# Optimization experiments

Measured on AMD Instinct MI355X. Metric: run time of the kernel, lower is better.

The kernel has to match this reference:

```python
import jax, jax.numpy as jnp
import numpy as np


def setup_inputs() -> dict:
    key = jax.random.key(0)
    ks = jax.random.split(key, 11)
    B, D, H = 2048, 1024, 1024
    return {
        "x": jax.random.normal(ks[0], (B, D), jnp.float32),
        "h_prev": jax.random.normal(ks[1], (B, H), jnp.float32),
        "W_mu": jax.random.normal(ks[2], (D, 3 * H), jnp.float32) * 0.05,
        "W_rho": jax.random.normal(ks[3], (D, 3 * H), jnp.float32) - 4.0,
        "U_mu": jax.random.normal(ks[4], (H, 3 * H), jnp.float32) * 0.05,
        "U_rho": jax.random.normal(ks[5], (H, 3 * H), jnp.float32) - 4.0,
        "b_mu": jax.random.normal(ks[6], (3 * H,), jnp.float32) * 0.05,
        "b_rho": jax.random.normal(ks[7], (3 * H,), jnp.float32) - 4.0,
        "r_eps": jax.random.normal(ks[8], (H,), jnp.float32),
        "u_eps": jax.random.normal(ks[9], (H,), jnp.float32),
        "h_pre_eps": jax.random.normal(ks[10], (H,), jnp.float32),
    }


def reference(x, h_prev, W_mu, W_rho, U_mu, U_rho, b_mu, b_rho,
              r_eps, u_eps, h_pre_eps):
    # Local reparameterization GRU cell (Bayes-by-Backprop).
    # Fused mean path: [B, 3H]
    mu = x @ W_mu + h_prev @ U_mu + b_mu
    # Variance path: E[x]^2 with sigma = softplus(rho); note original adds
    # b_sig (not squared) as in the source code.
    W_sig2 = jnp.square(jax.nn.softplus(W_rho))
    U_sig2 = jnp.square(jax.nn.softplus(U_rho))
    b_sig = jax.nn.softplus(b_rho)
    sig = jnp.square(x) @ W_sig2 + jnp.square(h_prev) @ U_sig2 + b_sig

    H = h_prev.shape[1]
    mu_r, mu_u, mu_h = mu[:, :H], mu[:, H:2 * H], mu[:, 2 * H:]
    sig_r, sig_u, sig_h = sig[:, :H], sig[:, H:2 * H], sig[:, 2 * H:]

    r = jax.nn.sigmoid(mu_r + sig_r * r_eps)  # computed as in source (unused in local path h update)
    u = jax.nn.sigmoid(mu_u + sig_u * u_eps)
    h_pre = jnp.tanh(mu_h + sig_h * h_pre_eps)
    h = u * h_prev + (1.0 - u) * h_pre
    return h
```

## Files before the change

kernel.cpp:

```cpp
#include <hip/hip_runtime.h>
#include <stdint.h>

#define BB 2048
#define DD 1024
#define HH 1024
#define KK 4096
#define NN 2048

typedef __bf16 bf16x8 __attribute__((ext_vector_type(8)));
typedef float  f32x4  __attribute__((ext_vector_type(4)));
typedef unsigned short u16x8 __attribute__((ext_vector_type(8)));

__device__ __forceinline__ unsigned short f2bf(float f) {
  union { float f; uint32_t u; } v; v.f = f;
  uint32_t r = (v.u + 0x7FFFu + ((v.u >> 16) & 1u)) >> 16;
  return (unsigned short)r;
}
__device__ __forceinline__ float bf2f(unsigned short u) {
  union { float f; uint32_t i; } v; v.i = ((uint32_t)u) << 16; return v.f;
}

__device__ __forceinline__ float softplus_f(float x) {
  return (x > 20.f) ? x : __logf(1.f + __expf(x));
}

__global__ __launch_bounds__(256) void prep_aw(const float* __restrict__ x,
                                               const float* __restrict__ h,
                                               unsigned short* __restrict__ A,
                                               const float* __restrict__ Wmu,
                                               const float* __restrict__ Wrho,
                                               const float* __restrict__ Umu,
                                               const float* __restrict__ Urho,
                                               const float* __restrict__ ueps,
                                               const float* __restrict__ heps,
                                               unsigned short* __restrict__ Wt) {
  __shared__ float tile[64][65];
  int bxx = blockIdx.x;
  if (bxx >= 2048) {
    int T = (bxx - 2048) * 256 + threadIdx.x;
    int m  = T >> 10;
    int k4 = (T & 1023) << 2;
    int region = k4 >> 10;
    int off = k4 & 1023;
    const float* src = (region & 1) ? h : x;
    float4 v = *(const float4*)(src + (size_t)m * 1024 + off);
    if (region >= 2) { v.x *= v.x; v.y *= v.y; v.z *= v.z; v.w *= v.w; }
    ushort4 o;
    o.x = f2bf(v.x); o.y = f2bf(v.y); o.z = f2bf(v.z); o.w = f2bf(v.w);
    *(ushort4*)(A + (size_t)m * KK + k4) = o;
    return;
  }
  int bx = bxx;
  int n0 = (bx & 31) * 64;
  int k0 = (bx >> 5) * 64;
  int t = threadIdx.x;

  const float* src; int rowbase; bool sig = (k0 >= 2048);
  if      (k0 < 1024) { src = Wmu;  rowbase = k0; }
  else if (k0 < 2048) { src = Umu;  rowbase = k0 - 1024; }
  else if (k0 < 3072) { src = Wrho; rowbase = k0 - 2048; }
  else                { src = Urho; rowbase = k0 - 3072; }

  int nn  = t & 63;
  int kk0 = t >> 6;
  int n   = n0 + nn;
  float eps = 0.f;
  if (sig) eps = (n < 1024) ? ueps[n] : heps[n - 1024];
#pragma unroll
  for (int p = 0; p < 16; ++p) {
    int kk = p * 4 + kk0;
    float v = src[(size_t)(rowbase + kk) * 3072 + 1024 + n];
    if (sig) { float s = softplus_f(v); v = s * s * eps; }
    tile[kk][nn] = v;
  }
  __syncthreads();
  int kkw = t & 63;
  int nw0 = t >> 6;
#pragma unroll
  for (int p = 0; p < 16; ++p) {
    int nn2 = p * 4 + nw0;
    Wt[(size_t)(n0 + nn2) * KK + k0 + kkw] = f2bf(tile[kkw][nn2]);
  }
}

__device__ __forceinline__ void gload16(const unsigned short* g, unsigned short* l) {
  __builtin_amdgcn_global_load_lds((const __attribute__((address_space(1))) void*)g,
                                   (__attribute__((address_space(3))) void*)l, 16, 0, 0);
}

#define LOFS(buf, ab, half, row, chunk) \
  ((buf) * 32768 + (ab) * 16384 + (half) * 8192 + (row) * 64 + (chunk) * 8)

#define BAR() { asm volatile("" ::: "memory"); __builtin_amdgcn_s_barrier(); \
                asm volatile("" ::: "memory"); }
#define WAITL() { asm volatile("s_waitcnt lgkmcnt(0)" ::: "memory"); \
                  __builtin_amdgcn_sched_barrier(0); }
#define VMC(N) { asm volatile("s_waitcnt vmcnt(" #N ")" ::: "memory"); }

template <int SPLITK>
__global__ __launch_bounds__(512, 2) void gemm256(const unsigned short* __restrict__ A,
                                                  const unsigned short* __restrict__ Bt,
                                                  unsigned short* __restrict__ Gb) {
  constexpr int KSTEPS = (KK / 64) / SPLITK;
  __shared__ __align__(16) unsigned short lds[65536];
  const int tid = threadIdx.x;
  const int bx  = blockIdx.x;
  const int tile = bx & 63;
  const int kz   = bx >> 6;
  const int m0 = (tile >> 3) * 256;
  const int n0 = (tile & 7) * 256;
  const int kt0 = kz * KSTEPS;
  const int lane = tid & 63;
  const int wid  = tid >> 6;
  const int wm  = wid >> 2;
  const int wn  = wid & 3;
  const int lr  = lane & 15;
  const int lk  = lane >> 4;
  const int swz = lr & 7;
  const int wnh = wn >> 1;
  const int wnr = (wn & 1) * 64;

  f32x4 acc[8][4];
#pragma unroll
  for (int i = 0; i < 8; ++i)
#pragma unroll
    for (int j = 0; j < 4; ++j) acc[i][j] = (f32x4)0.f;
  bf16x8 b[4][2], aA[2][2], aB[2][2];

#define STAGE(ab, half, tl) do { if ((tl) < KSTEPS) {                          \
    const unsigned short* gb = (ab) ? Bt : A;                                  \
    int p0 = (ab) ? n0 : m0;                                                   \
    unsigned short* ld = &lds[LOFS((tl) & 1, ab, half, 0, 0)];                 \
    _Pragma("unroll") for (int j = 0; j < 2; ++j) {                            \
      int f = j * 512 + tid; int row = f >> 3; int c8 = (f & 7) ^ (row & 7);   \
      gload16(gb + (size_t)(p0 + (half) * 128 + row) * KK                      \
                 + (size_t)(kt0 + (tl)) * 64 + c8 * 8, ld + f * 8);            \
    } } } while (0)

#define READ_B(bufc) do {                                                      \
    _Pragma("unroll") for (int fj = 0; fj < 4; ++fj)                           \
    _Pragma("unroll") for (int ks = 0; ks < 2; ++ks)                           \
      b[fj][ks] = *(const bf16x8*)&lds[LOFS(bufc, 1, wnh, wnr + fj * 16 + lr,  \
                                            (ks * 4 + lk) ^ swz)];             \
  } while (0)

#define READ_AQ(bufc, q, dst) do {                                             \
    _Pragma("unroll") for (int f2 = 0; f2 < 2; ++f2)                           \
    _Pragma("unroll") for (int ks = 0; ks < 2; ++ks)                           \
      dst[f2][ks] = *(const bf16x8*)&lds[LOFS(bufc, 0, wm,                     \
                      (q) * 32 + f2 * 16 + lr, (ks * 4 + lk) ^ swz)];          \
  } while (0)

#define MFMA_Q(q, asrc) do {                                                   \
    __builtin_amdgcn_s_setprio(1);                                             \
    _Pragma("unroll") for (int f2 = 0; f2 < 2; ++f2)                           \
    _Pragma("unroll") for (int fj = 0; fj < 4; ++fj)                           \
    _Pragma("unroll") for (int ks = 0; ks < 2; ++ks)                           \
      acc[(q) * 2 + f2][fj] = __builtin_amdgcn_mfma_f32_16x16x32_bf16(         \
          asrc[f2][ks], b[fj][ks], acc[(q) * 2 + f2][fj], 0, 0, 0);            \
    __builtin_amdgcn_s_setprio(0);                                             \
  } while (0)

  STAGE(0, 0, 0); STAGE(0, 1, 0); STAGE(1, 0, 0); STAGE(1, 1, 0);
  STAGE(1, 0, 1); STAGE(1, 1, 1); STAGE(0, 0, 1);
  VMC(6); BAR();
  READ_B(0); READ_AQ(0, 0, aA);

#pragma unroll 1
  for (int tc = 0; tc < KSTEPS; ++tc) {
    const int bufc = tc & 1;
    const int nbufc = bufc ^ 1;
    const bool last = (tc + 2 >= KSTEPS);
    READ_AQ(bufc, 1, aB);
    STAGE(0, 1, tc + 1);
    BAR(); MFMA_Q(0, aA); WAITL(); BAR();
    READ_AQ(bufc, 2, aA);
    STAGE(1, 0, tc + 2);
    BAR(); MFMA_Q(1, aB); WAITL(); BAR();
    READ_AQ(bufc, 3, aB);
    STAGE(1, 1, tc + 2);
    BAR(); MFMA_Q(2, aA); WAITL(); BAR();
    STAGE(0, 0, tc + 2);
    BAR(); MFMA_Q(3, aB);
    if (last) { VMC(0); } else { VMC(6); }
    if (tc + 1 < KSTEPS) { READ_B(nbufc); READ_AQ(nbufc, 0, aA); }
    BAR();
  }

  unsigned short* wl = &lds[wid * 8192];
#pragma unroll
  for (int fi = 0; fi < 8; ++fi)
#pragma unroll
    for (int fj = 0; fj < 4; ++fj) {
      int rowb = fi * 16 + lk * 4;
#pragma unroll
      for (int q = 0; q < 4; ++q) {
        int row  = rowb + q;
        int colw = fj * 16 + lr;
        int el   = (colw & 7) + ((((colw >> 3) ^ row) & 7) << 3);
        wl[row * 64 + el] = f2bf(acc[fi][fj][q]);
      }
    }
  __syncthreads();
  unsigned short* Gz = Gb + (size_t)kz * BB * NN;
  {
    const int rl = lane >> 3;
    const int c  = lane & 7;
#pragma unroll
    for (int i = 0; i < 16; ++i) {
      int r = i * 8 + rl;
      bf16x8 vv = *(const bf16x8*)&wl[r * 64 + (((c ^ r) & 7) << 3)];
      *(bf16x8*)&Gz[(size_t)(m0 + wm * 128 + r) * NN + n0 + wn * 64 + c * 8] = vv;
    }
  }
#undef STAGE
#undef READ_B
#undef READ_AQ
#undef MFMA_Q
}

template <int SPLITK>
__global__ __launch_bounds__(256) void epilogue(const unsigned short* __restrict__ Gb,
                                                const float* __restrict__ hprev,
                                                const float* __restrict__ bmu,
                                                const float* __restrict__ brho,
                                                const float* __restrict__ ueps,
                                                const float* __restrict__ heps,
                                                float* __restrict__ out) {
  int T = blockIdx.x * 256 + threadIdx.x;
  int m  = T >> 7;
  int j8 = (T & 127) << 3;
  float gu[8] = {0.f,0.f,0.f,0.f,0.f,0.f,0.f,0.f};
  float gh[8] = {0.f,0.f,0.f,0.f,0.f,0.f,0.f,0.f};
#pragma unroll
  for (int z = 0; z < SPLITK; ++z) {
    const unsigned short* Gz = Gb + (size_t)z * BB * NN;
    u16x8 a = *(const u16x8*)(Gz + (size_t)m * NN + j8);
    u16x8 c = *(const u16x8*)(Gz + (size_t)m * NN + 1024 + j8);
#pragma unroll
    for (int e = 0; e < 8; ++e) { gu[e] += bf2f(a[e]); gh[e] += bf2f(c[e]); }
  }
  float hp[8], bu[8], ru[8], bh[8], rh[8], ue[8], he[8];
  *(float4*)&hp[0] = *(const float4*)(hprev + (size_t)m * 1024 + j8);
  *(float4*)&hp[4] = *(const float4*)(hprev + (size_t)m * 1024 + j8 + 4);
  *(float4*)&bu[0] = *(const float4*)(bmu + 1024 + j8);
  *(float4*)&bu[4] = *(const float4*)(bmu + 1024 + j8 + 4);
  *(float4*)&ru[0] = *(const float4*)(brho + 1024 + j8);
  *(float4*)&ru[4] = *(const float4*)(brho + 1024 + j8 + 4);
  *(float4*)&bh[0] = *(const float4*)(bmu + 2048 + j8);
  *(float4*)&bh[4] = *(const float4*)(bmu + 2048 + j8 + 4);
  *(float4*)&rh[0] = *(const float4*)(brho + 2048 + j8);
  *(float4*)&rh[4] = *(const float4*)(brho + 2048 + j8 + 4);
  *(float4*)&ue[0] = *(const float4*)(ueps + j8);
  *(float4*)&ue[4] = *(const float4*)(ueps + j8 + 4);
  *(float4*)&he[0] = *(const float4*)(heps + j8);
  *(float4*)&he[4] = *(const float4*)(heps + j8 + 4);
  float o[8];
#pragma unroll
  for (int c = 0; c < 8; ++c) {
    float zu = gu[c] + bu[c] + softplus_f(ru[c]) * ue[c];
    float zh = gh[c] + bh[c] + softplus_f(rh[c]) * he[c];
    float u  = 1.f / (1.f + __expf(-zu));
    float e2 = __expf(2.f * zh);
    float th = 1.f - 2.f / (e2 + 1.f);
    o[c] = u * hp[c] + (1.f - u) * th;
  }
  *(float4*)(out + (size_t)m * 1024 + j8)     = *(const float4*)&o[0];
  *(float4*)(out + (size_t)m * 1024 + j8 + 4) = *(const float4*)&o[4];
}

extern "C" void kernel_launch(void* const* d_in, const int* in_sizes, int n_in,
                              void* d_out, int out_size, void* d_ws, size_t ws_size,
                              hipStream_t stream) {
  const float* x     = (const float*)d_in[0];
  const float* hprev = (const float*)d_in[1];
  const float* Wmu   = (const float*)d_in[2];
  const float* Wrho  = (const float*)d_in[3];
  const float* Umu   = (const float*)d_in[4];
  const float* Urho  = (const float*)d_in[5];
  const float* bmu   = (const float*)d_in[6];
  const float* brho  = (const float*)d_in[7];
  const float* ueps  = (const float*)d_in[9];
  const float* heps  = (const float*)d_in[10];
  float* out = (float*)d_out;

  size_t aw = (size_t)BB * KK * 2;
  size_t ww = (size_t)NN * KK * 2;
  size_t gw = (size_t)BB * NN * 2;
  unsigned short* Abf = (unsigned short*)d_ws;
  unsigned short* Wt  = (unsigned short*)((char*)d_ws + aw);
  unsigned short* Gb  = (unsigned short*)((char*)d_ws + aw + ww);

  int splitk = 1;
  if      (ws_size >= aw + ww + 4 * gw) splitk = 4;
  else if (ws_size >= aw + ww + 2 * gw) splitk = 2;

  prep_aw<<<10240, 256, 0, stream>>>(x, hprev, Abf, Wmu, Wrho, Umu, Urho,
                                     ueps, heps, Wt);
  if (splitk == 4) {
    gemm256<4><<<256, 512, 0, stream>>>(Abf, Wt, Gb);
    epilogue<4><<<1024, 256, 0, stream>>>(Gb, hprev, bmu, brho, ueps, heps, out);
  } else if (splitk == 2) {
    gemm256<2><<<128, 512, 0, stream>>>(Abf, Wt, Gb);
    epilogue<2><<<1024, 256, 0, stream>>>(Gb, hprev, bmu, brho, ueps, heps, out);
  } else {
    gemm256<1><<<64, 512, 0, stream>>>(Abf, Wt, Gb);
    epilogue<1><<<1024, 256, 0, stream>>>(Gb, hprev, bmu, brho, ueps, heps, out);
  }
}
```

Baseline: 69.81 us.

## Shrink GEMM tile to 128x256 with BK=32 triple buffering, vectorize weight transpose store

Reworks the bf16 GEMM: block tile drops from 256x256 to 128x256 and the K step from 64 to 32, with a 3-stage LDS ring instead of 2-stage double buffering. This doubles the grid, cuts LDS use and raises the occupancy hint to 4 blocks per CU, aiming to fill more CUs and hide latency. The cost is less data reuse per block and more barriers per unit of K. Separately, the weight-transpose prep now writes 8 bf16 values per 16-byte store instead of scalar 2-byte stores. The epilogue drops a __syncthreads, which relies on each wave touching only its own LDS region.

```diff
diff --git a/kernel.cpp b/kernel.cpp
--- a/kernel.cpp
+++ b/kernel.cpp
@@ -74,12 +74,15 @@
     tile[kk][nn] = v;
   }
   __syncthreads();
-  int kkw = t & 63;
-  int nw0 = t >> 6;
-#pragma unroll
-  for (int p = 0; p < 16; ++p) {
-    int nn2 = p * 4 + nw0;
-    Wt[(size_t)(n0 + nn2) * KK + k0 + kkw] = f2bf(tile[kkw][nn2]);
+#pragma unroll
+  for (int p = 0; p < 2; ++p) {
+    int idx = p * 256 + t;
+    int nw  = idx >> 3;
+    int oc  = idx & 7;
+    u16x8 o8;
+#pragma unroll
+    for (int e = 0; e < 8; ++e) o8[e] = f2bf(tile[oc * 8 + e][nw]);
+    *(u16x8*)&Wt[(size_t)(n0 + nw) * KK + k0 + oc * 8] = o8;
   }
 }
 
@@ -87,9 +90,6 @@
   __builtin_amdgcn_global_load_lds((const __attribute__((address_space(1))) void*)g,
                                    (__attribute__((address_space(3))) void*)l, 16, 0, 0);
 }
-
-#define LOFS(buf, ab, half, row, chunk) \
-  ((buf) * 32768 + (ab) * 16384 + (half) * 8192 + (row) * 64 + (chunk) * 8)
 
 #define BAR() { asm volatile("" ::: "memory"); __builtin_amdgcn_s_barrier(); \
                 asm volatile("" ::: "memory"); }
@@ -98,16 +98,17 @@
 #define VMC(N) { asm volatile("s_waitcnt vmcnt(" #N ")" ::: "memory"); }
 
 template <int SPLITK>
-__global__ __launch_bounds__(512, 2) void gemm256(const unsigned short* __restrict__ A,
+__global__ __launch_bounds__(512, 4) void gemm256(const unsigned short* __restrict__ A,
                                                   const unsigned short* __restrict__ Bt,
                                                   unsigned short* __restrict__ Gb) {
-  constexpr int KSTEPS = (KK / 64) / SPLITK;
-  __shared__ __align__(16) unsigned short lds[65536];
+  constexpr int KSTEPS = (KK / 32) / SPLITK;
+  static_assert(KSTEPS >= 4, "");
+  __shared__ __align__(16) unsigned short lds[36864];
   const int tid = threadIdx.x;
   const int bx  = blockIdx.x;
-  const int tile = bx & 63;
-  const int kz   = bx >> 6;
-  const int m0 = (tile >> 3) * 256;
+  const int tile = bx & 127;
+  const int kz   = bx >> 7;
+  const int m0 = (tile >> 3) * 128;
   const int n0 = (tile & 7) * 256;
   const int kt0 = kz * KSTEPS;
   const int lane = tid & 63;
@@ -116,107 +117,87 @@
   const int wn  = wid & 3;
   const int lr  = lane & 15;
   const int lk  = lane >> 4;
-  const int swz = lr & 7;
-  const int wnh = wn >> 1;
-  const int wnr = (wn & 1) * 64;
-
-  f32x4 acc[8][4];
-#pragma unroll
-  for (int i = 0; i < 8; ++i)
+  const int roct = lk ^ (lr & 3);
+
+  f32x4 acc[4][4];
+#pragma unroll
+  for (int i = 0; i < 4; ++i)
 #pragma unroll
     for (int j = 0; j < 4; ++j) acc[i][j] = (f32x4)0.f;
-  bf16x8 b[4][2], aA[2][2], aB[2][2];
-
-#define STAGE(ab, half, tl) do { if ((tl) < KSTEPS) {                          \
-    const unsigned short* gb = (ab) ? Bt : A;                                  \
-    int p0 = (ab) ? n0 : m0;                                                   \
-    unsigned short* ld = &lds[LOFS((tl) & 1, ab, half, 0, 0)];                 \
+
+#define STAGE3(tl, sbuf) do { if ((tl) < KSTEPS) {                             \
+    {                                                                          \
+      int c = tid;                                                \
+      int row = c >> 2, oc = (c & 3) ^ (row & 3);                              \
+      gload16(A + (size_t)(m0 + row) * KK + (size_t)(kt0 + (tl)) * 32 + oc * 8,\
+              &lds[(sbuf) * 12288 + c * 8]);                                   \
+    }                                                                          \
     _Pragma("unroll") for (int j = 0; j < 2; ++j) {                            \
-      int f = j * 512 + tid; int row = f >> 3; int c8 = (f & 7) ^ (row & 7);   \
-      gload16(gb + (size_t)(p0 + (half) * 128 + row) * KK                      \
-                 + (size_t)(kt0 + (tl)) * 64 + c8 * 8, ld + f * 8);            \
+      int cb = j * 512 + tid;                                     \
+      int row = cb >> 2, oc = (cb & 3) ^ (row & 3);                            \
+      gload16(Bt + (size_t)(n0 + row) * KK + (size_t)(kt0 + (tl)) * 32 + oc * 8,\
+              &lds[(sbuf) * 12288 + 4096 + cb * 8]);                           \
     } } } while (0)
 
-#define READ_B(bufc) do {                                                      \
-    _Pragma("unroll") for (int fj = 0; fj < 4; ++fj)                           \
-    _Pragma("unroll") for (int ks = 0; ks < 2; ++ks)                           \
-      b[fj][ks] = *(const bf16x8*)&lds[LOFS(bufc, 1, wnh, wnr + fj * 16 + lr,  \
-                                            (ks * 4 + lk) ^ swz)];             \
-  } while (0)
-
-#define READ_AQ(bufc, q, dst) do {                                             \
-    _Pragma("unroll") for (int f2 = 0; f2 < 2; ++f2)                           \
-    _Pragma("unroll") for (int ks = 0; ks < 2; ++ks)                           \
-      dst[f2][ks] = *(const bf16x8*)&lds[LOFS(bufc, 0, wm,                     \
-                      (q) * 32 + f2 * 16 + lr, (ks * 4 + lk) ^ swz)];          \
-  } while (0)
-
-#define MFMA_Q(q, asrc) do {                                                   \
-    __builtin_amdgcn_s_setprio(1);                                             \
-    _Pragma("unroll") for (int f2 = 0; f2 < 2; ++f2)                           \
-    _Pragma("unroll") for (int fj = 0; fj < 4; ++fj)                           \
-    _Pragma("unroll") for (int ks = 0; ks < 2; ++ks)                           \
-      acc[(q) * 2 + f2][fj] = __builtin_amdgcn_mfma_f32_16x16x32_bf16(         \
-          asrc[f2][ks], b[fj][ks], acc[(q) * 2 + f2][fj], 0, 0, 0);            \
-    __builtin_amdgcn_s_setprio(0);                                             \
-  } while (0)
-
-  STAGE(0, 0, 0); STAGE(0, 1, 0); STAGE(1, 0, 0); STAGE(1, 1, 0);
-  STAGE(1, 0, 1); STAGE(1, 1, 1); STAGE(0, 0, 1);
-  VMC(6); BAR();
-  READ_B(0); READ_AQ(0, 0, aA);
-
+  STAGE3(0, 0);
+  STAGE3(1, 1);
+  VMC(3); BAR();
+
+  int bufc = 0, sb = 2;
 #pragma unroll 1
   for (int tc = 0; tc < KSTEPS; ++tc) {
-    const int bufc = tc & 1;
-    const int nbufc = bufc ^ 1;
-    const bool last = (tc + 2 >= KSTEPS);
-    READ_AQ(bufc, 1, aB);
-    STAGE(0, 1, tc + 1);
-    BAR(); MFMA_Q(0, aA); WAITL(); BAR();
-    READ_AQ(bufc, 2, aA);
-    STAGE(1, 0, tc + 2);
-    BAR(); MFMA_Q(1, aB); WAITL(); BAR();
-    READ_AQ(bufc, 3, aB);
-    STAGE(1, 1, tc + 2);
-    BAR(); MFMA_Q(2, aA); WAITL(); BAR();
-    STAGE(0, 0, tc + 2);
-    BAR(); MFMA_Q(3, aB);
-    if (last) { VMC(0); } else { VMC(6); }
-    if (tc + 1 < KSTEPS) { READ_B(nbufc); READ_AQ(nbufc, 0, aA); }
+    bf16x8 a[4], b[4];
+#pragma unroll
+    for (int f = 0; f < 4; ++f) {
+      int row = wm * 64 + f * 16 + lr;
+      a[f] = *(const bf16x8*)&lds[bufc * 12288 + row * 32 + roct * 8];
+    }
+#pragma unroll
+    for (int f = 0; f < 4; ++f) {
+      int row = wn * 64 + f * 16 + lr;
+      b[f] = *(const bf16x8*)&lds[bufc * 12288 + 4096 + row * 32 + roct * 8];
+    }
+    STAGE3(tc + 2, sb);
+    BAR(); WAITL();
+    __builtin_amdgcn_s_setprio(1);
+#pragma unroll
+    for (int fi = 0; fi < 4; ++fi)
+#pragma unroll
+      for (int fj = 0; fj < 4; ++fj)
+        acc[fi][fj] = __builtin_amdgcn_mfma_f32_16x16x32_bf16(a[fi], b[fj],
+                                                              acc[fi][fj], 0, 0, 0);
+    __builtin_amdgcn_s_setprio(0);
+    if (tc + 3 <= KSTEPS) { VMC(3); } else { VMC(0); }
     BAR();
-  }
-
-  unsigned short* wl = &lds[wid * 8192];
-#pragma unroll
-  for (int fi = 0; fi < 8; ++fi)
+    bufc = (bufc == 2) ? 0 : bufc + 1;
+    sb   = (sb   == 2) ? 0 : sb   + 1;
+  }
+
+  unsigned short* wl = &lds[wid * 4096];
+#pragma unroll
+  for (int fi = 0; fi < 4; ++fi)
 #pragma unroll
     for (int fj = 0; fj < 4; ++fj) {
-      int rowb = fi * 16 + lk * 4;
 #pragma unroll
       for (int q = 0; q < 4; ++q) {
-        int row  = rowb + q;
-        int colw = fj * 16 + lr;
-        int el   = (colw & 7) + ((((colw >> 3) ^ row) & 7) << 3);
-        wl[row * 64 + el] = f2bf(acc[fi][fj][q]);
+        int row = fi * 16 + lk * 4 + q;
+        int col = fj * 16 + lr;
+        int oct = (col >> 3) ^ (row & 7);
+        wl[row * 64 + oct * 8 + (col & 7)] = f2bf(acc[fi][fj][q]);
       }
     }
-  __syncthreads();
   unsigned short* Gz = Gb + (size_t)kz * BB * NN;
   {
     const int rl = lane >> 3;
-    const int c  = lane & 7;
-#pragma unroll
-    for (int i = 0; i < 16; ++i) {
+    const int c8 = lane & 7;
+#pragma unroll
+    for (int i = 0; i < 8; ++i) {
       int r = i * 8 + rl;
-      bf16x8 vv = *(const bf16x8*)&wl[r * 64 + (((c ^ r) & 7) << 3)];
-      *(bf16x8*)&Gz[(size_t)(m0 + wm * 128 + r) * NN + n0 + wn * 64 + c * 8] = vv;
-    }
-  }
-#undef STAGE
-#undef READ_B
-#undef READ_AQ
-#undef MFMA_Q
+      bf16x8 vv = *(const bf16x8*)&wl[r * 64 + ((c8 ^ (r & 7)) * 8)];
+      *(bf16x8*)&Gz[(size_t)(m0 + wm * 64 + r) * NN + n0 + wn * 64 + c8 * 8] = vv;
+    }
+  }
+#undef STAGE3
 }
 
 template <int SPLITK>
@@ -298,13 +279,13 @@
   prep_aw<<<10240, 256, 0, stream>>>(x, hprev, Abf, Wmu, Wrho, Umu, Urho,
                                      ueps, heps, Wt);
   if (splitk == 4) {
-    gemm256<4><<<256, 512, 0, stream>>>(Abf, Wt, Gb);
+    gemm256<4><<<512, 512, 0, stream>>>(Abf, Wt, Gb);
     epilogue<4><<<1024, 256, 0, stream>>>(Gb, hprev, bmu, brho, ueps, heps, out);
   } else if (splitk == 2) {
-    gemm256<2><<<128, 512, 0, stream>>>(Abf, Wt, Gb);
+    gemm256<2><<<256, 512, 0, stream>>>(Abf, Wt, Gb);
     epilogue<2><<<1024, 256, 0, stream>>>(Gb, hprev, bmu, brho, ueps, heps, out);
   } else {
-    gemm256<1><<<64, 512, 0, stream>>>(Abf, Wt, Gb);
+    gemm256<1><<<128, 512, 0, stream>>>(Abf, Wt, Gb);
     epilogue<1><<<1024, 256, 0, stream>>>(Gb, hprev, bmu, brho, ueps, heps, out);
   }
 }
```

Measured after the change: 73.18 us. 4.8% more time.
